# Optimization experiments

Hardware: AMD Instinct MI355X
Metric: run time of the kernel (lower is better)

## Reference

```python
import jax, jax.numpy as jnp
import numpy as np

N = 20000      # nodes
E = 320000     # edges
G = 512        # graphs in batch
F_IN = 64      # node_feature_dim
SOLV = 128     # solvent fingerprint dim
OUT = 1        # output_dim
EPS = 1e-5     # BatchNorm eps


def setup_inputs() -> dict:
    key = jax.random.key(0)
    ks = jax.random.split(key, 24)
    inp = {
        'x': jax.random.normal(ks[0], (N, F_IN), jnp.float32),
        'edge_index': jax.random.randint(ks[1], (2, E), 0, N),
        'batch': jnp.sort(jax.random.randint(ks[2], (N,), 0, G)),
        'solvent_fingerprint': jax.random.normal(ks[3], (G, SOLV), jnp.float32),
        # GCNConv 1: 64 -> 128
        'W1': jax.random.normal(ks[4], (F_IN, 128), jnp.float32) / np.sqrt(F_IN),
        'b1': jnp.zeros((128,), jnp.float32),
        'g1': 1.0 + 0.1 * jax.random.normal(ks[5], (128,), jnp.float32),
        'be1': 0.1 * jax.random.normal(ks[6], (128,), jnp.float32),
        # GCNConv 2: 128 -> 256
        'W2': jax.random.normal(ks[7], (128, 256), jnp.float32) / np.sqrt(128),
        'b2': jnp.zeros((256,), jnp.float32),
        'g2': 1.0 + 0.1 * jax.random.normal(ks[8], (256,), jnp.float32),
        'be2': 0.1 * jax.random.normal(ks[9], (256,), jnp.float32),
        # fc_solvent: 128 -> 128
        'Ws': jax.random.normal(ks[10], (SOLV, 128), jnp.float32) / np.sqrt(SOLV),
        'bs': jnp.zeros((128,), jnp.float32),
        # fc1: 384 -> 128 (+ BN)
        'Wf1': jax.random.normal(ks[11], (384, 128), jnp.float32) / np.sqrt(384),
        'bf1': jnp.zeros((128,), jnp.float32),
        'gf1': 1.0 + 0.1 * jax.random.normal(ks[12], (128,), jnp.float32),
        'bef1': 0.1 * jax.random.normal(ks[13], (128,), jnp.float32),
        # fc2: 128 -> OUT
        'Wf2': jax.random.normal(ks[14], (128, OUT), jnp.float32) / np.sqrt(128),
        'bf2': jnp.zeros((OUT,), jnp.float32),
    }
    return inp


def _batchnorm(h, g, b):
    # training-mode BatchNorm1d: biased batch statistics
    mu = jnp.mean(h, axis=0)
    var = jnp.var(h, axis=0)
    return g * (h - mu) * jax.lax.rsqrt(var + EPS) + b


def _gcn_norm(edge_index, n_nodes):
    # add self-loops, symmetric normalization (PyG GCNConv default)
    loops = jnp.arange(n_nodes)
    row = jnp.concatenate([edge_index[0], loops])
    col = jnp.concatenate([edge_index[1], loops])
    deg = jax.ops.segment_sum(jnp.ones_like(col, jnp.float32), col, num_segments=n_nodes)
    dis = jax.lax.rsqrt(deg)  # deg >= 1 due to self-loops
    norm = dis[row] * dis[col]  # [E+N]
    return row, col, norm


def _gcn_conv(h, W, b, row, col, norm, n_nodes):
    hw = h @ W                                   # [N, F_out]
    msg = hw[row] * norm[:, None]                # gather + scale
    agg = jax.ops.segment_sum(msg, col, num_segments=n_nodes)
    return agg + b


def reference(x, edge_index, batch, solvent_fingerprint,
              W1, b1, g1, be1, W2, b2, g2, be2,
              Ws, bs, Wf1, bf1, gf1, bef1, Wf2, bf2):
    n = x.shape[0]
    row, col, norm = _gcn_norm(edge_index, n)

    h = jax.nn.relu(_batchnorm(_gcn_conv(x, W1, b1, row, col, norm, n), g1, be1))
    h = jax.nn.relu(_batchnorm(_gcn_conv(h, W2, b2, row, col, norm, n), g2, be2))

    # global_mean_pool
    sums = jax.ops.segment_sum(h, batch, num_segments=G)
    cnts = jax.ops.segment_sum(jnp.ones((n,), h.dtype), batch, num_segments=G)
    pooled = sums / jnp.maximum(cnts, 1.0)[:, None]          # [G, 256]

    solv = jax.nn.relu(solvent_fingerprint @ Ws + bs)        # [G, 128]
    z = jnp.concatenate([pooled, solv], axis=1)              # [G, 384]
    z = jax.nn.relu(_batchnorm(z @ Wf1 + bf1, gf1, bef1))    # dropout = identity (eval)
    return z @ Wf2 + bf2                                     # [G, OUT]
```

## Files before the change

### kernel.cpp

```cpp
#include <hip/hip_runtime.h>
#include <hip/hip_bf16.h>
#include <hip/hip_fp16.h>

#define EPS 1e-5f
#define CAP 64

typedef __attribute__((ext_vector_type(8))) short short8_t;
typedef __attribute__((ext_vector_type(8))) unsigned short ushort8_t;
typedef __attribute__((ext_vector_type(4))) float f32x4_t;

__device__ inline unsigned short f2bf(float f) {
    unsigned int u = __float_as_uint(f);
    unsigned int r = (u + 0x7FFFu + ((u >> 16) & 1u)) >> 16;
    return (unsigned short)r;
}
__device__ inline float bf2f(unsigned short h) {
    return __uint_as_float((unsigned int)h << 16);
}

__global__ void prep_kernel(const float* __restrict__ x, unsigned short* __restrict__ xb,
                            int* __restrict__ cursor, float* __restrict__ st,
                            const int* __restrict__ batch, int* __restrict__ seg,
                            float* __restrict__ out, const float* __restrict__ bf2,
                            int n, int G) {
    int i = blockIdx.x * blockDim.x + threadIdx.x;
    if (i < n * 8) {
        const float4* xf4 = (const float4*)x;
        float4 u = xf4[i * 2];
        float4 v = xf4[i * 2 + 1];
        ushort8_t h;
        h[0] = f2bf(u.x); h[1] = f2bf(u.y); h[2] = f2bf(u.z); h[3] = f2bf(u.w);
        h[4] = f2bf(v.x); h[5] = f2bf(v.y); h[6] = f2bf(v.z); h[7] = f2bf(v.w);
        ((ushort8_t*)xb)[i] = h;
    }
    if (i < n) cursor[i] = 0;
    if (i < 1028) st[i] = 0.f;
    if (i < G) out[i] = bf2[0];
    if (i <= G) {
        if (i == G) { seg[G] = n; }
        else {
            int lo = 0, hi = n;
            while (lo < hi) {
                int mid = (lo + hi) >> 1;
                if (batch[mid] < i) lo = mid + 1; else hi = mid;
            }
            seg[i] = lo;
        }
    }
}

__global__ void fillb_kernel(const int* __restrict__ ei, int* __restrict__ cursor,
                             unsigned int* __restrict__ recs, int E) {
    int e = blockIdx.x * blockDim.x + threadIdx.x;
    if (e >= E) return;
    int r = ei[e];
    int c = ei[E + e];
    int pos = atomicAdd(&cursor[c], 1);
    recs[(size_t)c * CAP + pos] = (unsigned int)r;
}

__global__ __launch_bounds__(256)
void gather1_pack_kernel(const unsigned short* __restrict__ xb,
                         const int* __restrict__ cursor,
                         unsigned int* __restrict__ recs,
                         unsigned short* __restrict__ dst,
                         int n, int gps, int GB1) {
    const int bid = blockIdx.x;
    const int t   = threadIdx.x;

    if (bid >= GB1) {
        int i = (bid - GB1) * 256 + t;
        int node = i >> 6;
        if (node < n && (i & 63) < cursor[node]) {
            unsigned int r = recs[i] & 0xFFFFu;
            float w = rsqrtf((float)cursor[r] + 1.0f);
            recs[i] = (((unsigned int)__half_as_ushort(__float2half_rn(w))) << 16) | r;
        }
        return;
    }

    int xl    = bid & 7;
    int slice = xl >> 2;
    int group = (bid >> 3) * 4 + (xl & 3);
    if (group >= gps) return;
    int local = t / 4;
    int lane  = t % 4;
    int node  = group * 64 + local;
    if (node >= n) return;
    int f8    = slice * 4 + lane;

    const ushort8_t* src8 = (const ushort8_t*)xb;
    int deg  = cursor[node];
    float di = rsqrtf((float)deg + 1.0f);
    ushort8_t sv = src8[(size_t)node * 8 + f8];
    float acc[8], acc2[8];
#pragma unroll
    for (int j = 0; j < 8; j++) { acc[j] = bf2f(sv[j]) * di; acc2[j] = 0.f; }

    int e  = node * CAP;
    int e1 = e + deg;
    for (; e + 1 < e1; e += 2) {
        int r0 = recs[e] & 0xFFFF;
        int r1 = recs[e + 1] & 0xFFFF;
        float w0 = rsqrtf((float)cursor[r0] + 1.0f);
        float w1 = rsqrtf((float)cursor[r1] + 1.0f);
        ushort8_t v0 = src8[(size_t)r0 * 8 + f8];
        ushort8_t v1 = src8[(size_t)r1 * 8 + f8];
#pragma unroll
        for (int j = 0; j < 8; j++) {
            acc[j]  = fmaf(bf2f(v0[j]), w0, acc[j]);
            acc2[j] = fmaf(bf2f(v1[j]), w1, acc2[j]);
        }
    }
    if (e < e1) {
        int r0 = recs[e] & 0xFFFF;
        float w0 = rsqrtf((float)cursor[r0] + 1.0f);
        ushort8_t v0 = src8[(size_t)r0 * 8 + f8];
#pragma unroll
        for (int j = 0; j < 8; j++) acc[j] = fmaf(bf2f(v0[j]), w0, acc[j]);
    }
    ushort8_t o;
#pragma unroll
    for (int j = 0; j < 8; j++) o[j] = f2bf((acc[j] + acc2[j]) * di);
    ((ushort8_t*)dst)[(size_t)node * 8 + f8] = o;
}

template <int F, bool BN>
__launch_bounds__(256)
__global__ void gather_kernel(const unsigned short* __restrict__ src,
                              const int* __restrict__ cursor,
                              const unsigned int* __restrict__ recs,
                              const float* __restrict__ st, const float* __restrict__ gamma,
                              const float* __restrict__ beta, float inv_n,
                              unsigned short* __restrict__ dst, int n, int gps) {
    constexpr int F8  = F / 8;
    constexpr int W8  = F8 / 2;
    constexpr int NPB = 256 / W8;

    int bid = blockIdx.x;
    int xl  = bid & 7;
    int slice = xl >> 2;
    int group = (bid >> 3) * 4 + (xl & 3);
    if (group >= gps) return;

    int local = threadIdx.x / W8;
    int lane  = threadIdx.x % W8;
    int node  = group * NPB + local;
    if (node >= n) return;
    int f8    = slice * W8 + lane;
    int feat0 = f8 * 8;

    float sc[8], sh[8];
    if (BN) {
#pragma unroll
        for (int j = 0; j < 8; j++) {
            float m = st[feat0 + j] * inv_n;
            float v = st[F + feat0 + j] * inv_n - m * m;
            sc[j] = gamma[feat0 + j] * rsqrtf(v + EPS);
            sh[j] = beta[feat0 + j] - m * sc[j];
        }
    }

    const ushort8_t* src8 = (const ushort8_t*)src;
    int deg  = cursor[node];
    float di = rsqrtf((float)deg + 1.0f);
    ushort8_t sv = src8[(size_t)node * F8 + f8];
    float acc[8], acc2[8];
#pragma unroll
    for (int j = 0; j < 8; j++) {
        float f = bf2f(sv[j]);
        if (BN) f = fmaxf(fmaf(f, sc[j], sh[j]), 0.f);
        acc[j]  = f * di;
        acc2[j] = 0.f;
    }

    int e  = node * CAP;
    int e1 = e + deg;
    for (; e + 3 < e1; e += 4) {
        unsigned int q0 = recs[e],     q1 = recs[e + 1];
        unsigned int q2 = recs[e + 2], q3 = recs[e + 3];
        int r0 = q0 & 0xFFFF, r1 = q1 & 0xFFFF;
        int r2 = q2 & 0xFFFF, r3 = q3 & 0xFFFF;
        float w0 = __half2float(__ushort_as_half((unsigned short)(q0 >> 16)));
        float w1 = __half2float(__ushort_as_half((unsigned short)(q1 >> 16)));
        float w2 = __half2float(__ushort_as_half((unsigned short)(q2 >> 16)));
        float w3 = __half2float(__ushort_as_half((unsigned short)(q3 >> 16)));
        ushort8_t v0 = src8[(size_t)r0 * F8 + f8];
        ushort8_t v1 = src8[(size_t)r1 * F8 + f8];
        ushort8_t v2 = src8[(size_t)r2 * F8 + f8];
        ushort8_t v3 = src8[(size_t)r3 * F8 + f8];
#pragma unroll
        for (int j = 0; j < 8; j++) {
            float f0 = bf2f(v0[j]);
            float f1 = bf2f(v1[j]);
            float f2 = bf2f(v2[j]);
            float f3 = bf2f(v3[j]);
            if (BN) {
                f0 = fmaxf(fmaf(f0, sc[j], sh[j]), 0.f);
                f1 = fmaxf(fmaf(f1, sc[j], sh[j]), 0.f);
                f2 = fmaxf(fmaf(f2, sc[j], sh[j]), 0.f);
                f3 = fmaxf(fmaf(f3, sc[j], sh[j]), 0.f);
            }
            acc[j]  = fmaf(f0, w0, acc[j]);
            acc2[j] = fmaf(f1, w1, acc2[j]);
            acc[j]  = fmaf(f2, w2, acc[j]);
            acc2[j] = fmaf(f3, w3, acc2[j]);
        }
    }
    for (; e < e1; e++) {
        unsigned int q0 = recs[e];
        int r0 = q0 & 0xFFFF;
        float w0 = __half2float(__ushort_as_half((unsigned short)(q0 >> 16)));
        ushort8_t v0 = src8[(size_t)r0 * F8 + f8];
#pragma unroll
        for (int j = 0; j < 8; j++) {
            float f0 = bf2f(v0[j]);
            if (BN) f0 = fmaxf(fmaf(f0, sc[j], sh[j]), 0.f);
            acc[j] = fmaf(f0, w0, acc[j]);
        }
    }
    ushort8_t o;
#pragma unroll
    for (int j = 0; j < 8; j++) o[j] = f2bf((acc[j] + acc2[j]) * di);
    ((ushort8_t*)dst)[(size_t)node * F8 + f8] = o;
}

template <int K, int NTOT, int OMODE, bool A_F32, bool STATS>
__device__ void gemm_body(char* smemc, int row0, int col0,
                          const void* __restrict__ A, int lda,
                          const float* __restrict__ B, const float* __restrict__ bias,
                          void* __restrict__ Cout, int ldc, float* __restrict__ st, int M) {
    constexpr int KP = K + 8;
    unsigned short (*As)[KP] = (unsigned short (*)[KP])smemc;
    unsigned short (*Bs)[KP] = (unsigned short (*)[KP])(smemc + (size_t)64 * KP * 2);
    float (*sred)[64][2]     = (float (*)[64][2])(smemc + (size_t)2 * 64 * KP * 2);

    const int t    = threadIdx.x;
    const int lane = t & 63;
    const int wave = t >> 6;
    const int wr   = wave >> 1;
    const int wc   = wave & 1;

    constexpr int PA = (64 * K / 8) / 256;
#pragma unroll
    for (int p = 0; p < PA; p++) {
        int fi = t + 256 * p;
        int r  = fi / (K / 8);
        int c8 = fi % (K / 8);
        ushort8_t v = {};
        if (row0 + r < M) {
            if (A_F32) {
                const float* Af = (const float*)A;
                float4 u0 = *(const float4*)&Af[(size_t)(row0 + r) * lda + c8 * 8];
                float4 u1 = *(const float4*)&Af[(size_t)(row0 + r) * lda + c8 * 8 + 4];
                v[0] = f2bf(u0.x); v[1] = f2bf(u0.y); v[2] = f2bf(u0.z); v[3] = f2bf(u0.w);
                v[4] = f2bf(u1.x); v[5] = f2bf(u1.y); v[6] = f2bf(u1.z); v[7] = f2bf(u1.w);
            } else {
                v = *(const ushort8_t*)&((const unsigned short*)A)[(size_t)(row0 + r) * lda + c8 * 8];
            }
        }
        *(ushort8_t*)&As[r][c8 * 8] = v;
    }
    constexpr int PB = (K * 16) / 256;
#pragma unroll
    for (int p = 0; p < PB; p++) {
        int fi = t + 256 * p;
        int k  = fi >> 4;
        int c4 = fi & 15;
        float4 v = *(const float4*)&B[(size_t)k * NTOT + col0 + c4 * 4];
        Bs[c4 * 4 + 0][k] = f2bf(v.x);
        Bs[c4 * 4 + 1][k] = f2bf(v.y);
        Bs[c4 * 4 + 2][k] = f2bf(v.z);
        Bs[c4 * 4 + 3][k] = f2bf(v.w);
    }
    __syncthreads();

    const int l15 = lane & 15;
    const int l16 = lane >> 4;
    f32x4_t acc[2][2] = {};
#pragma unroll
    for (int ks = 0; ks < K / 32; ks++) {
        int koff = ks * 32 + l16 * 8;
        short8_t a0 = *(const short8_t*)&As[wr * 32 + l15][koff];
        short8_t a1 = *(const short8_t*)&As[wr * 32 + 16 + l15][koff];
        short8_t b0 = *(const short8_t*)&Bs[wc * 32 + l15][koff];
        short8_t b1 = *(const short8_t*)&Bs[wc * 32 + 16 + l15][koff];
        acc[0][0] = __builtin_amdgcn_mfma_f32_16x16x32_bf16(a0, b0, acc[0][0], 0, 0, 0);
        acc[0][1] = __builtin_amdgcn_mfma_f32_16x16x32_bf16(a0, b1, acc[0][1], 0, 0, 0);
        acc[1][0] = __builtin_amdgcn_mfma_f32_16x16x32_bf16(a1, b0, acc[1][0], 0, 0, 0);
        acc[1][1] = __builtin_amdgcn_mfma_f32_16x16x32_bf16(a1, b1, acc[1][1], 0, 0, 0);
    }

    float s1[2] = {0.f, 0.f}, s2[2] = {0.f, 0.f};
#pragma unroll
    for (int m = 0; m < 2; m++) {
#pragma unroll
        for (int j = 0; j < 4; j++) {
            int row = row0 + wr * 32 + m * 16 + l16 * 4 + j;
            if (row < M) {
#pragma unroll
                for (int nn = 0; nn < 2; nn++) {
                    int col = col0 + wc * 32 + nn * 16 + l15;
                    float v = acc[m][nn][j] + bias[col];
                    if (OMODE == 2) v = fmaxf(v, 0.f);
                    if (OMODE == 0) ((float*)Cout)[(size_t)row * ldc + col] = v;
                    else ((unsigned short*)Cout)[(size_t)row * ldc + col] = f2bf(v);
                    if (STATS) { s1[nn] += v; s2[nn] += v * v; }
                }
            }
        }
    }
    if (STATS) {
#pragma unroll
        for (int nn = 0; nn < 2; nn++) {
            s1[nn] += __shfl_xor(s1[nn], 16);
            s1[nn] += __shfl_xor(s1[nn], 32);
            s2[nn] += __shfl_xor(s2[nn], 16);
            s2[nn] += __shfl_xor(s2[nn], 32);
        }
        if (lane < 16) {
#pragma unroll
            for (int nn = 0; nn < 2; nn++) {
                sred[wr][wc * 32 + nn * 16 + lane][0] = s1[nn];
                sred[wr][wc * 32 + nn * 16 + lane][1] = s2[nn];
            }
        }
        __syncthreads();
        if (t < 64) {
            float a = sred[0][t][0] + sred[1][t][0];
            float b = sred[0][t][1] + sred[1][t][1];
            atomicAdd(&st[col0 + t], a);
            atomicAdd(&st[NTOT + col0 + t], b);
        }
    }
}

__global__ __launch_bounds__(256)
void gemm1_solv_kernel(const unsigned short* __restrict__ a1b,
                       const float* __restrict__ W1, const float* __restrict__ b1,
                       unsigned short* __restrict__ h1b, float* __restrict__ st1,
                       const float* __restrict__ sf, const float* __restrict__ Ws,
                       const float* __restrict__ bs, unsigned short* __restrict__ zs,
                       int n, int g1b, int G) {
    __shared__ alignas(16) char smem[35840];
    int bid = blockIdx.x;
    if (bid < g1b) {
        int MT = g1b / 2;
        gemm_body<64, 128, 1, false, true>(smem, (bid % MT) * 64, (bid / MT) * 64,
                                           a1b, 64, W1, b1, h1b, 128, st1, n);
    } else {
        int s = bid - g1b;
        gemm_body<128, 128, 2, true, false>(smem, (s >> 1) * 64, (s & 1) * 64,
                                            sf, 128, Ws, bs, zs, 128, nullptr, G);
    }
}

__global__ __launch_bounds__(256)
void gemm2_kernel(const unsigned short* __restrict__ h1, const float* __restrict__ W2,
                  const float* __restrict__ b2, unsigned short* __restrict__ a2b,
                  float* __restrict__ st2, int n) {
    __shared__ alignas(16) char smem[35840];
    gemm_body<128, 256, 1, false, true>(smem, blockIdx.x * 64, blockIdx.y * 64,
                                        h1, 128, W2, b2, a2b, 256, st2, n);
}

__launch_bounds__(256)
__global__ void pool_kernel(const unsigned short* __restrict__ a2b, const int* __restrict__ seg,
                            const float* __restrict__ st2, const float* __restrict__ g2,
                            const float* __restrict__ be2, float inv_n,
                            unsigned short* __restrict__ z) {
    __shared__ float4 red[4][64];
    int g  = blockIdx.x;
    int t  = threadIdx.x;
    int r  = t >> 6;
    int f4 = t & 63;

    float4 sc, sh;
    {
        float m0 = st2[f4 * 4 + 0] * inv_n, m1 = st2[f4 * 4 + 1] * inv_n;
        float m2 = st2[f4 * 4 + 2] * inv_n, m3 = st2[f4 * 4 + 3] * inv_n;
        sc.x = g2[f4 * 4 + 0] * rsqrtf(st2[256 + f4 * 4 + 0] * inv_n - m0 * m0 + EPS);
        sc.y = g2[f4 * 4 + 1] * rsqrtf(st2[256 + f4 * 4 + 1] * inv_n - m1 * m1 + EPS);
        sc.z = g2[f4 * 4 + 2] * rsqrtf(st2[256 + f4 * 4 + 2] * inv_n - m2 * m2 + EPS);
        sc.w = g2[f4 * 4 + 3] * rsqrtf(st2[256 + f4 * 4 + 3] * inv_n - m3 * m3 + EPS);
        sh.x = be2[f4 * 4 + 0] - m0 * sc.x;
        sh.y = be2[f4 * 4 + 1] - m1 * sc.y;
        sh.z = be2[f4 * 4 + 2] - m2 * sc.z;
        sh.w = be2[f4 * 4 + 3] - m3 * sc.w;
    }

    int i0 = seg[g], i1 = seg[g + 1];
    float4 acc = make_float4(0.f, 0.f, 0.f, 0.f);
    for (int i = i0 + r; i < i1; i += 4) {
        ushort4 v = *(const ushort4*)&a2b[(size_t)i * 256 + f4 * 4];
        acc.x += fmaxf(fmaf(bf2f(v.x), sc.x, sh.x), 0.f);
        acc.y += fmaxf(fmaf(bf2f(v.y), sc.y, sh.y), 0.f);
        acc.z += fmaxf(fmaf(bf2f(v.z), sc.z, sh.z), 0.f);
        acc.w += fmaxf(fmaf(bf2f(v.w), sc.w, sh.w), 0.f);
    }
    red[r][f4] = acc;
    __syncthreads();
    if (t < 64) {
        float4 a = red[0][t], b = red[1][t], c = red[2][t], d = red[3][t];
        float inv = 1.0f / fmaxf((float)(i1 - i0), 1.f);
        ushort4 o;
        o.x = f2bf((a.x + b.x + c.x + d.x) * inv);
        o.y = f2bf((a.y + b.y + c.y + d.y) * inv);
        o.z = f2bf((a.z + b.z + c.z + d.z) * inv);
        o.w = f2bf((a.w + b.w + c.w + d.w) * inv);
        *(ushort4*)&z[(size_t)g * 256 + t * 4] = o;
    }
}

__global__ __launch_bounds__(256)
void head_kernel(const unsigned short* __restrict__ z, const unsigned short* __restrict__ zs,
                 const float* __restrict__ Wf1, const float* __restrict__ bf1,
                 const float* __restrict__ gf, const float* __restrict__ bef,
                 const float* __restrict__ Wf2,
                 float* __restrict__ stf, int* __restrict__ ctr,
                 float* __restrict__ out, float inv_g, int nblocks) {
    constexpr int KP = 136;
    __shared__ unsigned short As[64][KP];
    __shared__ unsigned short Bs[64][KP];
    __shared__ float sred[2][64][2];

    const int t    = threadIdx.x;
    const int lane = t & 63;
    const int wave = t >> 6;
    const int wr   = wave >> 1;
    const int wc   = wave & 1;
    const int row0 = (blockIdx.x >> 1) * 64;
    const int col0 = (blockIdx.x & 1) * 64;
    const int l15  = lane & 15;
    const int l16  = lane >> 4;

    f32x4_t acc[2][2] = {};
    for (int kc = 0; kc < 3; kc++) {
        __syncthreads();
#pragma unroll
        for (int p = 0; p < 4; p++) {
            int fi = t + 256 * p;
            int r  = fi >> 4, c8 = fi & 15;
            const unsigned short* ap = (kc < 2)
                ? &z[(size_t)(row0 + r) * 256 + kc * 128 + c8 * 8]
                : &zs[(size_t)(row0 + r) * 128 + c8 * 8];
            *(ushort8_t*)&As[r][c8 * 8] = *(const ushort8_t*)ap;
        }
#pragma unroll
        for (int p = 0; p < 8; p++) {
            int fi = t + 256 * p;
            int k  = fi >> 4, c4 = fi & 15;
            float4 v = *(const float4*)&Wf1[(size_t)(kc * 128 + k) * 128 + col0 + c4 * 4];
            Bs[c4 * 4 + 0][k] = f2bf(v.x);
            Bs[c4 * 4 + 1][k] = f2bf(v.y);
            Bs[c4 * 4 + 2][k] = f2bf(v.z);
            Bs[c4 * 4 + 3][k] = f2bf(v.w);
        }
        __syncthreads();
#pragma unroll
        for (int ks = 0; ks < 4; ks++) {
            int koff = ks * 32 + l16 * 8;
            short8_t a0 = *(const short8_t*)&As[wr * 32 + l15][koff];
            short8_t a1 = *(const short8_t*)&As[wr * 32 + 16 + l15][koff];
            short8_t b0 = *(const short8_t*)&Bs[wc * 32 + l15][koff];
            short8_t b1 = *(const short8_t*)&Bs[wc * 32 + 16 + l15][koff];
            acc[0][0] = __builtin_amdgcn_mfma_f32_16x16x32_bf16(a0, b0, acc[0][0], 0, 0, 0);
            acc[0][1] = __builtin_amdgcn_mfma_f32_16x16x32_bf16(a0, b1, acc[0][1], 0, 0, 0);
            acc[1][0] = __builtin_amdgcn_mfma_f32_16x16x32_bf16(a1, b0, acc[1][0], 0, 0, 0);
            acc[1][1] = __builtin_amdgcn_mfma_f32_16x16x32_bf16(a1, b1, acc[1][1], 0, 0, 0);
        }
    }

    float s1[2] = {0.f, 0.f}, s2[2] = {0.f, 0.f};
#pragma unroll
    for (int m = 0; m < 2; m++)
#pragma unroll
        for (int j = 0; j < 4; j++)
#pragma unroll
            for (int nn = 0; nn < 2; nn++) {
                int col = col0 + wc * 32 + nn * 16 + l15;
                float v = acc[m][nn][j] + bf1[col];
                acc[m][nn][j] = v;
                s1[nn] += v;
                s2[nn] += v * v;
            }
#pragma unroll
    for (int nn = 0; nn < 2; nn++) {
        s1[nn] += __shfl_xor(s1[nn], 16);
        s1[nn] += __shfl_xor(s1[nn], 32);
        s2[nn] += __shfl_xor(s2[nn], 16);
        s2[nn] += __shfl_xor(s2[nn], 32);
    }
    if (lane < 16) {
#pragma unroll
        for (int nn = 0; nn < 2; nn++) {
            sred[wr][wc * 32 + nn * 16 + lane][0] = s1[nn];
            sred[wr][wc * 32 + nn * 16 + lane][1] = s2[nn];
        }
    }
    __syncthreads();
    if (t < 64) {
        atomicAdd(&stf[col0 + t],       sred[0][t][0] + sred[1][t][0]);
        atomicAdd(&stf[128 + col0 + t], sred[0][t][1] + sred[1][t][1]);
    }

    __threadfence();
    __syncthreads();
    if (t == 0) {
        atomicAdd(ctr, 1);
        while (atomicAdd(ctr, 0) < nblocks) { }
    }
    __syncthreads();

    float* sflat = &sred[0][0][0];
    sflat[t] = atomicAdd(&stf[t], 0.f);
    __syncthreads();

#pragma unroll
    for (int m = 0; m < 2; m++)
#pragma unroll
        for (int j = 0; j < 4; j++) {
            float p = 0.f;
#pragma unroll
            for (int nn = 0; nn < 2; nn++) {
                int col = col0 + wc * 32 + nn * 16 + l15;
                float mean = sflat[col] * inv_g;
                float var  = sflat[128 + col] * inv_g - mean * mean;
                float sc   = gf[col] * rsqrtf(var + EPS);
                float sh   = bef[col] - mean * sc;
                p += fmaxf(fmaf(acc[m][nn][j], sc, sh), 0.f) * Wf2[col];
            }
            p += __shfl_xor(p, 1);
            p += __shfl_xor(p, 2);
            p += __shfl_xor(p, 4);
            p += __shfl_xor(p, 8);
            if (l15 == 0) {
                int row = wr * 32 + m * 16 + l16 * 4 + j;
                atomicAdd(&out[row0 + row], p);
            }
        }
}

extern "C" void kernel_launch(void* const* d_in, const int* in_sizes, int n_in,
                              void* d_out, int out_size, void* d_ws, size_t ws_size,
                              hipStream_t stream) {
    const float* x    = (const float*)d_in[0];
    const int*   ei   = (const int*)d_in[1];
    const int*   batch= (const int*)d_in[2];
    const float* sf   = (const float*)d_in[3];
    const float* W1   = (const float*)d_in[4];
    const float* b1   = (const float*)d_in[5];
    const float* g1   = (const float*)d_in[6];
    const float* be1  = (const float*)d_in[7];
    const float* W2   = (const float*)d_in[8];
    const float* b2   = (const float*)d_in[9];
    const float* g2   = (const float*)d_in[10];
    const float* be2  = (const float*)d_in[11];
    const float* Ws   = (const float*)d_in[12];
    const float* bs   = (const float*)d_in[13];
    const float* Wf1  = (const float*)d_in[14];
    const float* bf1  = (const float*)d_in[15];
    const float* gf1  = (const float*)d_in[16];
    const float* bef1 = (const float*)d_in[17];
    const float* Wf2  = (const float*)d_in[18];
    const float* bf2  = (const float*)d_in[19];
    float* out = (float*)d_out;

    const int n = in_sizes[0] / 64;
    const int E = in_sizes[1] / 2;
    const int G = in_sizes[3] / 128;

    float* ws = (float*)d_ws;
    unsigned short* a2b = (unsigned short*)ws;
    unsigned short* xb  = (unsigned short*)(ws + (size_t)n * 128);
    unsigned short* a1b = (unsigned short*)(ws + (size_t)n * 160);
    unsigned short* h1b = (unsigned short*)(ws + (size_t)n * 224);
    unsigned short* z   = (unsigned short*)(ws + (size_t)n * 288);
    unsigned short* zs  = (unsigned short*)(ws + (size_t)n * 288 + (size_t)G * 128);
    float* st   = ws + (size_t)n * 288 + (size_t)G * 192;
    float* st1  = st;
    float* st2  = st + 256;
    float* stf  = st + 768;
    int*   ctr  = (int*)(st + 1024);
    int*   cursor = (int*)(st + 1028);
    int*   seg    = cursor + n;
    unsigned int* recs = (unsigned int*)(seg + G + 1);

    const float inv_nn = 1.0f / (float)n;
    const float inv_gg = 1.0f / (float)G;
    const int MT = (n + 63) / 64;

    prep_kernel<<<(n * 8 + 255) / 256, 256, 0, stream>>>(x, xb, cursor, st, batch, seg,
                                                         out, bf2, n, G);
    fillb_kernel<<<(E + 255) / 256, 256, 0, stream>>>(ei, cursor, recs, E);

    {
        int gps = (n + 63) / 64;
        int GB1 = ((gps + 3) / 4) * 8;
        int PB  = (n * CAP + 255) / 256;
        gather1_pack_kernel<<<GB1 + PB, 256, 0, stream>>>(xb, cursor, recs, a1b, n, gps, GB1);
    }

    gemm1_solv_kernel<<<MT * 2 + (G / 64) * 2, 256, 0, stream>>>(
        a1b, W1, b1, h1b, st1, sf, Ws, bs, zs, n, MT * 2, G);

    {
        int gps = (n + 31) / 32;
        int grid = ((gps + 3) / 4) * 8;
        gather_kernel<128, true><<<grid, 256, 0, stream>>>(
            h1b, cursor, recs, st1, g1, be1, inv_nn, a1b, n, gps);
    }

    gemm2_kernel<<<dim3(MT, 4), 256, 0, stream>>>(a1b, W2, b2, a2b, st2, n);

    pool_kernel<<<G, 256, 0, stream>>>(a2b, seg, st2, g2, be2, inv_nn, z);

    head_kernel<<<(G / 64) * 2, 256, 0, stream>>>(z, zs, Wf1, bf1, gf1, bef1, Wf2,
                                                  stf, ctr, out, inv_gg, (G / 64) * 2);
}
```

Baseline: 115.2 us.

## Assign one wavefront per node and split edges across lanes in GCN gathers

Both neighbor-aggregation kernels now give each node a full 64-lane wave. The node's edge list is strided across lane subgroups (16 subgroups for the 64-feature layer, 8 for the 128-feature layer), and partial sums are combined with xor shuffles. The goal is to fix the load imbalance and serialized per-thread edge loops of the old thread-per-node-slice mapping, and to expose more memory-level parallelism for the random gathers. In exchange it adds shuffle-reduction work, launches many more blocks, and leaves most lanes idle for low-degree nodes.

Result: slower. 127.3 us (+10.5%).

```diff
diff --git a/kernel.cpp b/kernel.cpp
--- a/kernel.cpp
+++ b/kernel.cpp
@@ -83,71 +83,61 @@
     int slice = xl >> 2;
     int group = (bid >> 3) * 4 + (xl & 3);
     if (group >= gps) return;
-    int local = t / 4;
-    int lane  = t % 4;
-    int node  = group * 64 + local;
+    int wave = t >> 6;
+    int lane = t & 63;
+    int node = group * 4 + wave;
     if (node >= n) return;
-    int f8    = slice * 4 + lane;
+    int esub = lane >> 2;
+    int f8   = (lane & 3) + slice * 4;
 
     const ushort8_t* src8 = (const ushort8_t*)xb;
     int deg  = cursor[node];
     float di = rsqrtf((float)deg + 1.0f);
-    ushort8_t sv = src8[(size_t)node * 8 + f8];
-    float acc[8], acc2[8];
-#pragma unroll
-    for (int j = 0; j < 8; j++) { acc[j] = bf2f(sv[j]) * di; acc2[j] = 0.f; }
-
-    int e  = node * CAP;
-    int e1 = e + deg;
-    for (; e + 1 < e1; e += 2) {
-        int r0 = recs[e] & 0xFFFF;
-        int r1 = recs[e + 1] & 0xFFFF;
-        float w0 = rsqrtf((float)cursor[r0] + 1.0f);
-        float w1 = rsqrtf((float)cursor[r1] + 1.0f);
-        ushort8_t v0 = src8[(size_t)r0 * 8 + f8];
-        ushort8_t v1 = src8[(size_t)r1 * 8 + f8];
-#pragma unroll
-        for (int j = 0; j < 8; j++) {
-            acc[j]  = fmaf(bf2f(v0[j]), w0, acc[j]);
-            acc2[j] = fmaf(bf2f(v1[j]), w1, acc2[j]);
-        }
-    }
-    if (e < e1) {
-        int r0 = recs[e] & 0xFFFF;
-        float w0 = rsqrtf((float)cursor[r0] + 1.0f);
-        ushort8_t v0 = src8[(size_t)r0 * 8 + f8];
-#pragma unroll
-        for (int j = 0; j < 8; j++) acc[j] = fmaf(bf2f(v0[j]), w0, acc[j]);
-    }
-    ushort8_t o;
-#pragma unroll
-    for (int j = 0; j < 8; j++) o[j] = f2bf((acc[j] + acc2[j]) * di);
-    ((ushort8_t*)dst)[(size_t)node * 8 + f8] = o;
-}
-
-template <int F, bool BN>
-__launch_bounds__(256)
-__global__ void gather_kernel(const unsigned short* __restrict__ src,
-                              const int* __restrict__ cursor,
-                              const unsigned int* __restrict__ recs,
-                              const float* __restrict__ st, const float* __restrict__ gamma,
-                              const float* __restrict__ beta, float inv_n,
-                              unsigned short* __restrict__ dst, int n, int gps) {
-    constexpr int F8  = F / 8;
-    constexpr int W8  = F8 / 2;
-    constexpr int NPB = 256 / W8;
-
+    float acc[8] = {};
+    int base = node * CAP;
+    for (int it = esub; it < deg; it += 16) {
+        int r = recs[base + it] & 0xFFFF;
+        float w = rsqrtf((float)cursor[r] + 1.0f);
+        ushort8_t v = src8[(size_t)r * 8 + f8];
+#pragma unroll
+        for (int j = 0; j < 8; j++) acc[j] = fmaf(bf2f(v[j]), w, acc[j]);
+    }
+#pragma unroll
+    for (int j = 0; j < 8; j++) {
+        acc[j] += __shfl_xor(acc[j], 4);
+        acc[j] += __shfl_xor(acc[j], 8);
+        acc[j] += __shfl_xor(acc[j], 16);
+        acc[j] += __shfl_xor(acc[j], 32);
+    }
+    if (esub == 0) {
+        ushort8_t sv = src8[(size_t)node * 8 + f8];
+        ushort8_t o;
+#pragma unroll
+        for (int j = 0; j < 8; j++) o[j] = f2bf((acc[j] + bf2f(sv[j]) * di) * di);
+        ((ushort8_t*)dst)[(size_t)node * 8 + f8] = o;
+    }
+}
+
+template <bool BN>
+__global__ __launch_bounds__(256)
+void gather2_kernel(const unsigned short* __restrict__ src,
+                    const int* __restrict__ cursor,
+                    const unsigned int* __restrict__ recs,
+                    const float* __restrict__ st, const float* __restrict__ gamma,
+                    const float* __restrict__ beta, float inv_n,
+                    unsigned short* __restrict__ dst, int n, int gps) {
     int bid = blockIdx.x;
-    int xl  = bid & 7;
+    int xl    = bid & 7;
     int slice = xl >> 2;
     int group = (bid >> 3) * 4 + (xl & 3);
     if (group >= gps) return;
-
-    int local = threadIdx.x / W8;
-    int lane  = threadIdx.x % W8;
-    int node  = group * NPB + local;
+    int t    = threadIdx.x;
+    int wave = t >> 6;
+    int lane = t & 63;
+    int node = group * 4 + wave;
     if (node >= n) return;
-    int f8    = slice * W8 + lane;
+    int esub = lane >> 3;
+    int f8   = (lane & 7) + slice * 8;
     int feat0 = f8 * 8;
 
     float sc[8], sh[8];
@@ -155,7 +145,7 @@
 #pragma unroll
         for (int j = 0; j < 8; j++) {
             float m = st[feat0 + j] * inv_n;
-            float v = st[F + feat0 + j] * inv_n - m * m;
+            float v = st[128 + feat0 + j] * inv_n - m * m;
             sc[j] = gamma[feat0 + j] * rsqrtf(v + EPS);
             sh[j] = beta[feat0 + j] - m * sc[j];
         }
@@ -164,65 +154,37 @@
     const ushort8_t* src8 = (const ushort8_t*)src;
     int deg  = cursor[node];
     float di = rsqrtf((float)deg + 1.0f);
-    ushort8_t sv = src8[(size_t)node * F8 + f8];
-    float acc[8], acc2[8];
+    float acc[8] = {};
+    int base = node * CAP;
+    for (int it = esub; it < deg; it += 8) {
+        unsigned int q = recs[base + it];
+        int r = q & 0xFFFF;
+        float w = __half2float(__ushort_as_half((unsigned short)(q >> 16)));
+        ushort8_t v = src8[(size_t)r * 16 + f8];
+#pragma unroll
+        for (int j = 0; j < 8; j++) {
+            float f = bf2f(v[j]);
+            if (BN) f = fmaxf(fmaf(f, sc[j], sh[j]), 0.f);
+            acc[j] = fmaf(f, w, acc[j]);
+        }
+    }
 #pragma unroll
     for (int j = 0; j < 8; j++) {
-        float f = bf2f(sv[j]);
-        if (BN) f = fmaxf(fmaf(f, sc[j], sh[j]), 0.f);
-        acc[j]  = f * di;
-        acc2[j] = 0.f;
-    }
-
-    int e  = node * CAP;
-    int e1 = e + deg;
-    for (; e + 3 < e1; e += 4) {
-        unsigned int q0 = recs[e],     q1 = recs[e + 1];
-        unsigned int q2 = recs[e + 2], q3 = recs[e + 3];
-        int r0 = q0 & 0xFFFF, r1 = q1 & 0xFFFF;
-        int r2 = q2 & 0xFFFF, r3 = q3 & 0xFFFF;
-        float w0 = __half2float(__ushort_as_half((unsigned short)(q0 >> 16)));
-        float w1 = __half2float(__ushort_as_half((unsigned short)(q1 >> 16)));
-        float w2 = __half2float(__ushort_as_half((unsigned short)(q2 >> 16)));
-        float w3 = __half2float(__ushort_as_half((unsigned short)(q3 >> 16)));
-        ushort8_t v0 = src8[(size_t)r0 * F8 + f8];
-        ushort8_t v1 = src8[(size_t)r1 * F8 + f8];
-        ushort8_t v2 = src8[(size_t)r2 * F8 + f8];
-        ushort8_t v3 = src8[(size_t)r3 * F8 + f8];
+        acc[j] += __shfl_xor(acc[j], 8);
+        acc[j] += __shfl_xor(acc[j], 16);
+        acc[j] += __shfl_xor(acc[j], 32);
+    }
+    if (esub == 0) {
+        ushort8_t sv = src8[(size_t)node * 16 + f8];
+        ushort8_t o;
 #pragma unroll
         for (int j = 0; j < 8; j++) {
-            float f0 = bf2f(v0[j]);
-            float f1 = bf2f(v1[j]);
-            float f2 = bf2f(v2[j]);
-            float f3 = bf2f(v3[j]);
-            if (BN) {
-                f0 = fmaxf(fmaf(f0, sc[j], sh[j]), 0.f);
-                f1 = fmaxf(fmaf(f1, sc[j], sh[j]), 0.f);
-                f2 = fmaxf(fmaf(f2, sc[j], sh[j]), 0.f);
-                f3 = fmaxf(fmaf(f3, sc[j], sh[j]), 0.f);
-            }
-            acc[j]  = fmaf(f0, w0, acc[j]);
-            acc2[j] = fmaf(f1, w1, acc2[j]);
-            acc[j]  = fmaf(f2, w2, acc[j]);
-            acc2[j] = fmaf(f3, w3, acc2[j]);
-        }
-    }
-    for (; e < e1; e++) {
-        unsigned int q0 = recs[e];
-        int r0 = q0 & 0xFFFF;
-        float w0 = __half2float(__ushort_as_half((unsigned short)(q0 >> 16)));
-        ushort8_t v0 = src8[(size_t)r0 * F8 + f8];
-#pragma unroll
-        for (int j = 0; j < 8; j++) {
-            float f0 = bf2f(v0[j]);
-            if (BN) f0 = fmaxf(fmaf(f0, sc[j], sh[j]), 0.f);
-            acc[j] = fmaf(f0, w0, acc[j]);
-        }
-    }
-    ushort8_t o;
-#pragma unroll
-    for (int j = 0; j < 8; j++) o[j] = f2bf((acc[j] + acc2[j]) * di);
-    ((ushort8_t*)dst)[(size_t)node * F8 + f8] = o;
+            float f = bf2f(sv[j]);
+            if (BN) f = fmaxf(fmaf(f, sc[j], sh[j]), 0.f);
+            o[j] = f2bf((acc[j] + f * di) * di);
+        }
+        ((ushort8_t*)dst)[(size_t)node * 16 + f8] = o;
+    }
 }
 
 template <int K, int NTOT, int OMODE, bool A_F32, bool STATS>
@@ -595,7 +557,7 @@
     fillb_kernel<<<(E + 255) / 256, 256, 0, stream>>>(ei, cursor, recs, E);
 
     {
-        int gps = (n + 63) / 64;
+        int gps = (n + 3) / 4;
         int GB1 = ((gps + 3) / 4) * 8;
         int PB  = (n * CAP + 255) / 256;
         gather1_pack_kernel<<<GB1 + PB, 256, 0, stream>>>(xb, cursor, recs, a1b, n, gps, GB1);
@@ -605,9 +567,9 @@
         a1b, W1, b1, h1b, st1, sf, Ws, bs, zs, n, MT * 2, G);
 
     {
-        int gps = (n + 31) / 32;
+        int gps = (n + 3) / 4;
         int grid = ((gps + 3) / 4) * 8;
-        gather_kernel<128, true><<<grid, 256, 0, stream>>>(
+        gather2_kernel<true><<<grid, 256, 0, stream>>>(
             h1b, cursor, recs, st1, g1, be1, inv_nn, a1b, n, gps);
     }
 
```
